# Kernel optimization log

Measured on AMD Instinct MI355X. Metric: run time of the kernel, lower is better.

## Reference

```python
import jax, jax.numpy as jnp
import numpy as np

B, C, HID, H, W_ = 16, 2048, 256, 32, 32

def setup_inputs() -> dict:
    key = jax.random.key(0)
    k1, k2, k3 = jax.random.split(key, 3)
    return {
        "query_features": jax.random.normal(k1, (B, C, H, W_), dtype=jnp.float32),
        "prompt_features": jax.random.normal(k2, (B, C, H, W_), dtype=jnp.float32),
        "W": jax.random.normal(k3, (HID, C), dtype=jnp.float32) * 0.02,
        "b": jnp.zeros((HID,), dtype=jnp.float32),
    }

def reference(query_features, prompt_features, W, b):
    Bq, Cc, Hh, Ww = query_features.shape
    HW = Hh * Ww
    # 1x1 conv == channel matmul
    Q = jnp.einsum('oc,bchw->bohw', W, query_features) + b[None, :, None, None]
    K = jnp.einsum('oc,bchw->bohw', W, prompt_features) + b[None, :, None, None]
    Qf = Q.reshape(Bq, -1, HW)          # (b, hid, HW1)
    Kf = K.reshape(Bq, -1, HW)          # (b, hid, HW2)
    Vf = prompt_features.reshape(Bq, Cc, HW)  # (b, C, HW2)
    scores = jnp.einsum('bcq,bck->bqk', Qf, Kf)   # (b, HW1, HW2)
    A = jax.nn.softmax(scores, axis=-1)
    aligned = jnp.einsum('bqk,bck->bcq', A, Vf).reshape(Bq, Cc, Hh, Ww)
    # fusion_policy == 'cat'
    return jnp.concatenate([query_features, aligned], axis=1)
```

## Files before the change

### kernel.cpp

```cpp
#include <hip/hip_runtime.h>

#define NB   16
#define NC   2048
#define NHID 256
#define NHW  1024

using half4_t  = __attribute__((ext_vector_type(4))) _Float16;
using half8_t  = __attribute__((ext_vector_type(8))) _Float16;
using float4_t = __attribute__((ext_vector_type(4))) float;

#define OUT_BATCH_BYTES ((size_t)(4096u * 1024u) * 4u)

__device__ __forceinline__ void async_load16(const void* g, void* l) {
    __builtin_amdgcn_global_load_lds((__attribute__((address_space(1))) void*)g,
                                     (__attribute__((address_space(3))) void*)l, 16, 0, 0);
}

template <int NROWS>
__device__ __forceinline__ void stage_async(const _Float16* __restrict__ src, size_t stride_h,
                                            _Float16* __restrict__ lds, int t) {
    #pragma unroll
    for (int i = 0; i < NROWS / 32; ++i) {
        const int o   = i * 4096 + t * 16;
        const int row = o >> 7;
        const int s   = ((o >> 4) & 7) ^ (row & 7);
        const _Float16* g = src + (size_t)row * stride_h + s * 8;
        async_load16(g, (char*)lds + o);
    }
}

__device__ __forceinline__ half8_t frag_read(const _Float16* __restrict__ lds, int row, int kk, int quad) {
    const int s = (kk * 4 + quad) ^ (row & 7);
    return *(const half8_t*)((const char*)lds + row * 128 + s * 16);
}

#define ACC_INIT(acc) \
    _Pragma("unroll") for (int i_ = 0; i_ < 4; ++i_) \
    _Pragma("unroll") for (int j_ = 0; j_ < 4; ++j_) \
    _Pragma("unroll") for (int r_ = 0; r_ < 4; ++r_) acc[i_][j_][r_] = 0.f;

__device__ __forceinline__ void gemm_f16(const _Float16* __restrict__ A, size_t lda,
                                         const _Float16* __restrict__ B, size_t ldb,
                                         int K, _Float16* __restrict__ As, _Float16* __restrict__ Bs,
                                         float4_t acc[4][4]) {
    const int t = threadIdx.x;
    const int l = t & 63, quad = l >> 4, l15 = l & 15;
    const int w = t >> 6;
    const int wr = (w >> 1) * 64, wc = (w & 1) * 64;
    for (int k0 = 0; k0 < K; k0 += 64) {
        stage_async<128>(A + k0, lda, As, t);
        stage_async<128>(B + k0, ldb, Bs, t);
        __syncthreads();
        #pragma unroll
        for (int kk = 0; kk < 2; ++kk) {
            half8_t af[4], bf[4];
            #pragma unroll
            for (int i = 0; i < 4; ++i) af[i] = frag_read(As, wr + i * 16 + l15, kk, quad);
            #pragma unroll
            for (int j = 0; j < 4; ++j) bf[j] = frag_read(Bs, wc + j * 16 + l15, kk, quad);
            #pragma unroll
            for (int i = 0; i < 4; ++i)
                #pragma unroll
                for (int j = 0; j < 4; ++j)
                    acc[i][j] = __builtin_amdgcn_mfma_f32_16x16x32_f16(af[i], bf[j], acc[i][j], 0, 0, 0);
        }
        __syncthreads();
    }
}

__global__ __launch_bounds__(256) void prep_v_kernel(const float* __restrict__ pf,
                                                     float* __restrict__ out) {
    const int idx = blockIdx.x * 256 + threadIdx.x;
    const int b = idx >> 18;
    const int r = idx & 0x3FFFF;
    const float* src = pf + ((size_t)b << 21) + (size_t)r * 8;
    float4 a = *(const float4*)src;
    float4 c = *(const float4*)(src + 4);
    half8_t h;
    h[0] = (_Float16)a.x; h[1] = (_Float16)a.y; h[2] = (_Float16)a.z; h[3] = (_Float16)a.w;
    h[4] = (_Float16)c.x; h[5] = (_Float16)c.y; h[6] = (_Float16)c.z; h[7] = (_Float16)c.w;
    _Float16* dst = (_Float16*)((char*)out + (size_t)b * OUT_BATCH_BYTES) + (size_t)r * 8;
    *(half8_t*)dst = h;
}

__global__ __launch_bounds__(256) void wcvt_kernel(const float* __restrict__ W, _Float16* __restrict__ W16) {
    const int idx = (blockIdx.x * 256 + threadIdx.x) * 8;
    float4 a = *(const float4*)(W + idx);
    float4 c = *(const float4*)(W + idx + 4);
    half8_t h;
    h[0] = (_Float16)a.x; h[1] = (_Float16)a.y; h[2] = (_Float16)a.z; h[3] = (_Float16)a.w;
    h[4] = (_Float16)c.x; h[5] = (_Float16)c.y; h[6] = (_Float16)c.z; h[7] = (_Float16)c.w;
    *(half8_t*)(W16 + idx) = h;
}

__global__ __launch_bounds__(256) void proj16_kernel(
    const float* __restrict__ qf, const float* __restrict__ pf,
    const _Float16* __restrict__ W16, const float* __restrict__ bias,
    _Float16* __restrict__ Q16, _Float16* __restrict__ K16,
    float* __restrict__ out) {
    __shared__ __attribute__((aligned(16))) _Float16 As[64 * 72];
    __shared__ __attribute__((aligned(16))) _Float16 Bs[256 * 64];
    const int z = blockIdx.z, which = z >> 4, b = z & 15;
    const float* X = (which ? pf : qf) + (size_t)b * NC * NHW;
    float* passq = (float*)((char*)out + (size_t)b * OUT_BATCH_BYTES);
    _Float16* O = (which ? K16 : Q16) + (size_t)b * NHW * NHID;
    const int m0 = blockIdx.x * 64;
    const int t = threadIdx.x;
    const int l = t & 63, quad = l >> 4, l15 = l & 15;
    const int w = t >> 6;
    const int wc = w * 64;
    const int j = t & 15;
    const int g = t >> 4;

    float4_t acc[4][4];
    ACC_INIT(acc)

    for (int k0 = 0; k0 < NC; k0 += 64) {
        float4 xr[4];
        #pragma unroll
        for (int r = 0; r < 4; ++r)
            xr[r] = *(const float4*)(X + (size_t)(k0 + g * 4 + r) * NHW + m0 + j * 4);
        if (which == 0 && k0 >= 1024) {
            #pragma unroll
            for (int r = 0; r < 4; ++r)
                *(float4*)(passq + (size_t)(k0 + g * 4 + r) * NHW + m0 + j * 4) = xr[r];
        }
        #pragma unroll
        for (int e = 0; e < 4; ++e) {
            half4_t h;
            h[0] = (_Float16)((&xr[0].x)[e]);
            h[1] = (_Float16)((&xr[1].x)[e]);
            h[2] = (_Float16)((&xr[2].x)[e]);
            h[3] = (_Float16)((&xr[3].x)[e]);
            *(half4_t*)(As + (j * 4 + e) * 72 + g * 4) = h;
        }
        stage_async<256>(W16 + k0, NC, Bs, t);
        __syncthreads();
        #pragma unroll
        for (int kk = 0; kk < 2; ++kk) {
            half8_t af[4], bf[4];
            #pragma unroll
            for (int i = 0; i < 4; ++i)
                af[i] = *(const half8_t*)(As + (i * 16 + l15) * 72 + kk * 32 + quad * 8);
            #pragma unroll
            for (int jj = 0; jj < 4; ++jj)
                bf[jj] = frag_read(Bs, wc + jj * 16 + l15, kk, quad);
            #pragma unroll
            for (int i = 0; i < 4; ++i)
                #pragma unroll
                for (int jj = 0; jj < 4; ++jj)
                    acc[i][jj] = __builtin_amdgcn_mfma_f32_16x16x32_f16(af[i], bf[jj], acc[i][jj], 0, 0, 0);
        }
        __syncthreads();
    }
    #pragma unroll
    for (int jj = 0; jj < 4; ++jj) {
        const float bv = bias[wc + jj * 16 + l15];
        #pragma unroll
        for (int i = 0; i < 4; ++i)
            #pragma unroll
            for (int r = 0; r < 4; ++r) {
                int hw  = m0 + i * 16 + quad * 4 + r;
                int hid = wc + jj * 16 + l15;
                O[(size_t)hw * NHID + hid] = (_Float16)(acc[i][jj][r] + bv);
            }
    }
}

__global__ __launch_bounds__(256) void scores16_kernel(
    const _Float16* __restrict__ Q16, const _Float16* __restrict__ K16, float* __restrict__ S) {
    __shared__ __attribute__((aligned(16))) _Float16 As[8192];
    __shared__ __attribute__((aligned(16))) _Float16 Bs[8192];
    const int oid = blockIdx.x + blockIdx.y * 8 + blockIdx.z * 64;
    const int xcd = oid & 7, half = (oid >> 9) & 1, r = (oid >> 3) & 63;
    const int b = xcd * 2 + half;
    const int m0 = (r >> 3) * 128, n0 = (r & 7) * 128;
    float* Sb = S + (size_t)b * NHW * NHW;
    float4_t acc[4][4];
    ACC_INIT(acc)
    gemm_f16(Q16 + (size_t)b * NHW * NHID + (size_t)m0 * NHID, NHID,
             K16 + (size_t)b * NHW * NHID + (size_t)n0 * NHID, NHID, NHID, As, Bs, acc);
    const int t = threadIdx.x, l = t & 63, quad = l >> 4, l15 = l & 15, w = t >> 6;
    const int wr = (w >> 1) * 64, wc = (w & 1) * 64;
    #pragma unroll
    for (int i = 0; i < 4; ++i)
        #pragma unroll
        for (int j = 0; j < 4; ++j)
            #pragma unroll
            for (int rr = 0; rr < 4; ++rr) {
                int q1 = m0 + wr + i * 16 + quad * 4 + rr;
                int q2 = n0 + wc + j * 16 + l15;
                Sb[(size_t)q1 * NHW + q2] = acc[i][j][rr];
            }
}

__global__ __launch_bounds__(256) void softmax_kernel(float* __restrict__ S) {
    const int t = threadIdx.x, wave = t >> 6, lane = t & 63;
    float* row = S + ((size_t)blockIdx.x * 4 + wave) * NHW;
    float4 v[4];
    float mx = -1e30f;
    #pragma unroll
    for (int j = 0; j < 4; ++j) {
        v[j] = *(const float4*)(row + (lane << 2) + (j << 8));
        mx = fmaxf(mx, fmaxf(fmaxf(v[j].x, v[j].y), fmaxf(v[j].z, v[j].w)));
    }
    #pragma unroll
    for (int off = 32; off >= 1; off >>= 1) mx = fmaxf(mx, __shfl_xor(mx, off, 64));
    float s = 0.f;
    #pragma unroll
    for (int j = 0; j < 4; ++j) {
        v[j].x = __expf(v[j].x - mx); v[j].y = __expf(v[j].y - mx);
        v[j].z = __expf(v[j].z - mx); v[j].w = __expf(v[j].w - mx);
        s += v[j].x + v[j].y + v[j].z + v[j].w;
    }
    #pragma unroll
    for (int off = 32; off >= 1; off >>= 1) s += __shfl_xor(s, off, 64);
    const float inv = 1.0f / s;
    __syncthreads();
    _Float16* o = (_Float16*)row;
    #pragma unroll
    for (int j = 0; j < 4; ++j) {
        half4_t h;
        h[0] = (_Float16)(v[j].x * inv); h[1] = (_Float16)(v[j].y * inv);
        h[2] = (_Float16)(v[j].z * inv); h[3] = (_Float16)(v[j].w * inv);
        *(half4_t*)(o + (lane << 2) + (j << 8)) = h;
    }
}

__global__ __launch_bounds__(256) void av16_kernel(
    const float* __restrict__ S, float* __restrict__ out) {
    __shared__ __attribute__((aligned(16))) _Float16 As[8192];
    __shared__ __attribute__((aligned(16))) _Float16 Bs[8192];
    const int oid = blockIdx.x + blockIdx.y * 8 + blockIdx.z * 128;
    const int xcd = oid & 7, half = (oid >> 10) & 1, r = (oid >> 3) & 127;
    const int b = xcd * 2 + half;
    const int m0 = (r >> 3) * 128;
    const int n0 = (r & 7) * 128;
    const _Float16* Vb  = (const _Float16*)((const char*)out + (size_t)b * OUT_BATCH_BYTES);
    const _Float16* A16 = (const _Float16*)(S + (size_t)b * NHW * NHW);
    float* Ob = out + (size_t)b * (2 * NC) * NHW + (size_t)NC * NHW;
    float4_t acc[4][4];
    ACC_INIT(acc)
    gemm_f16(Vb + (size_t)m0 * NHW, NHW, A16 + (size_t)n0 * 2048, 2048, NHW, As, Bs, acc);
    const int t = threadIdx.x, l = t & 63, quad = l >> 4, l15 = l & 15, w = t >> 6;
    const int wr = (w >> 1) * 64, wc = (w & 1) * 64;
    #pragma unroll
    for (int i = 0; i < 4; ++i)
        #pragma unroll
        for (int j = 0; j < 4; ++j)
            #pragma unroll
            for (int rr = 0; rr < 4; ++rr) {
                int c = m0 + wr + i * 16 + quad * 4 + rr;
                int q = n0 + wc + j * 16 + l15;
                Ob[(size_t)c * NHW + q] = acc[i][j][rr];
            }
}

__global__ __launch_bounds__(256) void copy2_kernel(const uint4* __restrict__ qf,
                                                    uint4* __restrict__ out) {
    const int idx = blockIdx.x * 256 + threadIdx.x;
    const int b = idx >> 18;
    const int r = idx & 0x3FFFF;
    out[((size_t)b << 20) + r] = qf[((size_t)b << 19) + r];
}

extern "C" void kernel_launch(void* const* d_in, const int* in_sizes, int n_in,
                              void* d_out, int out_size, void* d_ws, size_t ws_size,
                              hipStream_t stream) {
    const float* qf   = (const float*)d_in[0];
    const float* pf   = (const float*)d_in[1];
    const float* Wm   = (const float*)d_in[2];
    const float* bias = (const float*)d_in[3];
    float* out = (float*)d_out;

    float*    S   = (float*)d_ws;
    _Float16* Q16 = (_Float16*)((char*)d_ws + ((size_t)64 << 20));
    _Float16* K16 = (_Float16*)((char*)d_ws + ((size_t)72 << 20));
    _Float16* W16 = (_Float16*)((char*)out + ((size_t)8 << 20));

    wcvt_kernel<<<256, 256, 0, stream>>>(Wm, W16);
    prep_v_kernel<<<16384, 256, 0, stream>>>(pf, out);
    proj16_kernel<<<dim3(16, 1, 32), 256, 0, stream>>>(qf, pf, W16, bias, Q16, K16, out);
    scores16_kernel<<<dim3(8, 8, 16), 256, 0, stream>>>(Q16, K16, S);
    softmax_kernel<<<NB * 256, 256, 0, stream>>>(S);
    av16_kernel<<<dim3(8, 16, 16), 256, 0, stream>>>(S, out);
    copy2_kernel<<<16384, 256, 0, stream>>>((const uint4*)qf, (uint4*)out);
}
```

Before: 652.3 us.

## Fuse V fp16 conversion into projection kernel and widen it to 512 threads

Removes the separate prep_v kernel by having the projection kernel write the fp16 copy of prompt features into the output scratch area while it already reads them. The projection block grows to 512 threads with 8 waves, each wave handling a 32x64 tile, and each thread loads two channel rows instead of four. This avoids a second full read of prompt features and one kernel launch, at the cost of more store traffic inside the projection kernel and a different occupancy profile.

Measured after the change: 612.5 us. 6.1% less time.

```diff
diff --git a/kernel.cpp b/kernel.cpp
--- a/kernel.cpp
+++ b/kernel.cpp
@@ -5,6 +5,7 @@
 #define NHID 256
 #define NHW  1024
 
+using half2_t  = __attribute__((ext_vector_type(2))) _Float16;
 using half4_t  = __attribute__((ext_vector_type(4))) _Float16;
 using half8_t  = __attribute__((ext_vector_type(8))) _Float16;
 using float4_t = __attribute__((ext_vector_type(4))) float;
@@ -22,6 +23,18 @@
     #pragma unroll
     for (int i = 0; i < NROWS / 32; ++i) {
         const int o   = i * 4096 + t * 16;
+        const int row = o >> 7;
+        const int s   = ((o >> 4) & 7) ^ (row & 7);
+        const _Float16* g = src + (size_t)row * stride_h + s * 8;
+        async_load16(g, (char*)lds + o);
+    }
+}
+
+__device__ __forceinline__ void stage_async512(const _Float16* __restrict__ src, size_t stride_h,
+                                               _Float16* __restrict__ lds, int t) {
+    #pragma unroll
+    for (int i = 0; i < 4; ++i) {
+        const int o   = i * 8192 + t * 16;
         const int row = o >> 7;
         const int s   = ((o >> 4) & 7) ^ (row & 7);
         const _Float16* g = src + (size_t)row * stride_h + s * 8;
@@ -68,21 +81,6 @@
     }
 }
 
-__global__ __launch_bounds__(256) void prep_v_kernel(const float* __restrict__ pf,
-                                                     float* __restrict__ out) {
-    const int idx = blockIdx.x * 256 + threadIdx.x;
-    const int b = idx >> 18;
-    const int r = idx & 0x3FFFF;
-    const float* src = pf + ((size_t)b << 21) + (size_t)r * 8;
-    float4 a = *(const float4*)src;
-    float4 c = *(const float4*)(src + 4);
-    half8_t h;
-    h[0] = (_Float16)a.x; h[1] = (_Float16)a.y; h[2] = (_Float16)a.z; h[3] = (_Float16)a.w;
-    h[4] = (_Float16)c.x; h[5] = (_Float16)c.y; h[6] = (_Float16)c.z; h[7] = (_Float16)c.w;
-    _Float16* dst = (_Float16*)((char*)out + (size_t)b * OUT_BATCH_BYTES) + (size_t)r * 8;
-    *(half8_t*)dst = h;
-}
-
 __global__ __launch_bounds__(256) void wcvt_kernel(const float* __restrict__ W, _Float16* __restrict__ W16) {
     const int idx = (blockIdx.x * 256 + threadIdx.x) * 8;
     float4 a = *(const float4*)(W + idx);
@@ -93,7 +91,7 @@
     *(half8_t*)(W16 + idx) = h;
 }
 
-__global__ __launch_bounds__(256) void proj16_kernel(
+__global__ __launch_bounds__(512, 4) void proj16_kernel(
     const float* __restrict__ qf, const float* __restrict__ pf,
     const _Float16* __restrict__ W16, const float* __restrict__ bias,
     _Float16* __restrict__ Q16, _Float16* __restrict__ K16,
@@ -102,51 +100,58 @@
     __shared__ __attribute__((aligned(16))) _Float16 Bs[256 * 64];
     const int z = blockIdx.z, which = z >> 4, b = z & 15;
     const float* X = (which ? pf : qf) + (size_t)b * NC * NHW;
-    float* passq = (float*)((char*)out + (size_t)b * OUT_BATCH_BYTES);
+    float*     passq = (float*)((char*)out + (size_t)b * OUT_BATCH_BYTES);
+    _Float16*  V16   = (_Float16*)((char*)out + (size_t)b * OUT_BATCH_BYTES);
     _Float16* O = (which ? K16 : Q16) + (size_t)b * NHW * NHID;
     const int m0 = blockIdx.x * 64;
     const int t = threadIdx.x;
     const int l = t & 63, quad = l >> 4, l15 = l & 15;
     const int w = t >> 6;
-    const int wc = w * 64;
-    const int j = t & 15;
-    const int g = t >> 4;
-
-    float4_t acc[4][4];
-    ACC_INIT(acc)
+    const int wr = (w >> 2) * 32;
+    const int wc = (w & 3) * 64;
+    const int j  = t & 15;
+    const int gs = t >> 4;
+
+    float4_t acc[2][4];
+    #pragma unroll
+    for (int i = 0; i < 2; ++i)
+        #pragma unroll
+        for (int jj = 0; jj < 4; ++jj)
+            #pragma unroll
+            for (int r = 0; r < 4; ++r) acc[i][jj][r] = 0.f;
 
     for (int k0 = 0; k0 < NC; k0 += 64) {
-        float4 xr[4];
-        #pragma unroll
-        for (int r = 0; r < 4; ++r)
-            xr[r] = *(const float4*)(X + (size_t)(k0 + g * 4 + r) * NHW + m0 + j * 4);
-        if (which == 0 && k0 >= 1024) {
-            #pragma unroll
-            for (int r = 0; r < 4; ++r)
-                *(float4*)(passq + (size_t)(k0 + g * 4 + r) * NHW + m0 + j * 4) = xr[r];
+        const int c0 = k0 + gs * 2;
+        float4 x0 = *(const float4*)(X + (size_t)c0 * NHW + m0 + j * 4);
+        float4 x1 = *(const float4*)(X + (size_t)(c0 + 1) * NHW + m0 + j * 4);
+        half4_t hv0, hv1;
+        #pragma unroll
+        for (int e = 0; e < 4; ++e) { hv0[e] = (_Float16)((&x0.x)[e]); hv1[e] = (_Float16)((&x1.x)[e]); }
+        if (which) {
+            *(half4_t*)(V16 + (size_t)c0 * NHW + m0 + j * 4)       = hv0;
+            *(half4_t*)(V16 + (size_t)(c0 + 1) * NHW + m0 + j * 4) = hv1;
+        } else if (k0 >= 1024) {
+            *(float4*)(passq + (size_t)c0 * NHW + m0 + j * 4)       = x0;
+            *(float4*)(passq + (size_t)(c0 + 1) * NHW + m0 + j * 4) = x1;
         }
         #pragma unroll
         for (int e = 0; e < 4; ++e) {
-            half4_t h;
-            h[0] = (_Float16)((&xr[0].x)[e]);
-            h[1] = (_Float16)((&xr[1].x)[e]);
-            h[2] = (_Float16)((&xr[2].x)[e]);
-            h[3] = (_Float16)((&xr[3].x)[e]);
-            *(half4_t*)(As + (j * 4 + e) * 72 + g * 4) = h;
-        }
-        stage_async<256>(W16 + k0, NC, Bs, t);
+            half2_t h2; h2[0] = hv0[e]; h2[1] = hv1[e];
+            *(half2_t*)(As + (j * 4 + e) * 72 + gs * 2) = h2;
+        }
+        stage_async512(W16 + k0, NC, Bs, t);
         __syncthreads();
         #pragma unroll
         for (int kk = 0; kk < 2; ++kk) {
-            half8_t af[4], bf[4];
-            #pragma unroll
-            for (int i = 0; i < 4; ++i)
-                af[i] = *(const half8_t*)(As + (i * 16 + l15) * 72 + kk * 32 + quad * 8);
+            half8_t af[2], bf[4];
+            #pragma unroll
+            for (int i = 0; i < 2; ++i)
+                af[i] = *(const half8_t*)(As + (wr + i * 16 + l15) * 72 + kk * 32 + quad * 8);
             #pragma unroll
             for (int jj = 0; jj < 4; ++jj)
                 bf[jj] = frag_read(Bs, wc + jj * 16 + l15, kk, quad);
             #pragma unroll
-            for (int i = 0; i < 4; ++i)
+            for (int i = 0; i < 2; ++i)
                 #pragma unroll
                 for (int jj = 0; jj < 4; ++jj)
                     acc[i][jj] = __builtin_amdgcn_mfma_f32_16x16x32_f16(af[i], bf[jj], acc[i][jj], 0, 0, 0);
@@ -157,10 +162,10 @@
     for (int jj = 0; jj < 4; ++jj) {
         const float bv = bias[wc + jj * 16 + l15];
         #pragma unroll
-        for (int i = 0; i < 4; ++i)
+        for (int i = 0; i < 2; ++i)
             #pragma unroll
             for (int r = 0; r < 4; ++r) {
-                int hw  = m0 + i * 16 + quad * 4 + r;
+                int hw  = m0 + wr + i * 16 + quad * 4 + r;
                 int hid = wc + jj * 16 + l15;
                 O[(size_t)hw * NHID + hid] = (_Float16)(acc[i][jj][r] + bv);
             }
@@ -279,8 +284,7 @@
     _Float16* W16 = (_Float16*)((char*)out + ((size_t)8 << 20));
 
     wcvt_kernel<<<256, 256, 0, stream>>>(Wm, W16);
-    prep_v_kernel<<<16384, 256, 0, stream>>>(pf, out);
-    proj16_kernel<<<dim3(16, 1, 32), 256, 0, stream>>>(qf, pf, W16, bias, Q16, K16, out);
+    proj16_kernel<<<dim3(16, 1, 32), 512, 0, stream>>>(qf, pf, W16, bias, Q16, K16, out);
     scores16_kernel<<<dim3(8, 8, 16), 256, 0, stream>>>(Q16, K16, S);
     softmax_kernel<<<NB * 256, 256, 0, stream>>>(S);
     av16_kernel<<<dim3(8, 16, 16), 256, 0, stream>>>(S, out);
```
